# Kernel tuning notes

Measured on AMD Instinct MI355X. Metric: run time of the kernel, lower is better.

## Reference

```python
import jax, jax.numpy as jnp
import numpy as np

EPS = 1e-3  # keras LayerNormalization default epsilon


def _layernorm(x, gamma, beta):
    mu = jnp.mean(x, axis=-1, keepdims=True)
    var = jnp.mean(jnp.square(x - mu), axis=-1, keepdims=True)
    return (x - mu) * jax.lax.rsqrt(var + EPS) * gamma + beta


def setup_inputs() -> dict:
    key = jax.random.key(0)
    B, T, D, H = 8, 2048, 192, 3
    KD = D           # TalkingHeadsAttention(key_dim=dim, value_dim=dim)
    HID = 4 * D      # mlp_ratio = 4.0
    ks = jax.random.split(key, 12)
    s_in = 0.02
    inp = {
        "x": jax.random.normal(ks[0], (B, T, D), jnp.float32),
        # norm1 / norm2
        "gamma1": jnp.ones((D,), jnp.float32),
        "beta1": jnp.zeros((D,), jnp.float32),
        "gamma2": jnp.ones((D,), jnp.float32),
        "beta2": jnp.zeros((D,), jnp.float32),
        # attention projections (qkv_bias=False -> no biases)
        "wq": jax.random.normal(ks[1], (D, H, KD), jnp.float32) * s_in,
        "wk": jax.random.normal(ks[2], (D, H, KD), jnp.float32) * s_in,
        "wv": jax.random.normal(ks[3], (D, H, KD), jnp.float32) * s_in,
        "wo": jax.random.normal(ks[4], (H, KD, D), jnp.float32) * s_in,
        # talking-heads mixing matrices [H, H]
        "pre_w": jnp.eye(H, dtype=jnp.float32) + jax.random.normal(ks[5], (H, H), jnp.float32) * 0.02,
        "post_w": jnp.eye(H, dtype=jnp.float32) + jax.random.normal(ks[6], (H, H), jnp.float32) * 0.02,
        # MLP (bias=True)
        "w1": jax.random.normal(ks[7], (D, HID), jnp.float32) * s_in,
        "b1": jnp.zeros((HID,), jnp.float32),
        "w2": jax.random.normal(ks[8], (HID, D), jnp.float32) * s_in,
        "b2": jnp.zeros((D,), jnp.float32),
    }
    return inp


def reference(x, gamma1, beta1, gamma2, beta2, wq, wk, wv, wo, pre_w, post_w, w1, b1, w2, b2):
    KD = wq.shape[-1]
    # --- pre-norm + talking-heads attention ---
    n = _layernorm(x, gamma1, beta1)                      # [B,T,D]
    q = jnp.einsum("btd,dhk->bthk", n, wq)               # [B,T,H,KD]
    k = jnp.einsum("bsd,dhk->bshk", n, wk)
    v = jnp.einsum("bsd,dhk->bshk", n, wv)
    scores = jnp.einsum("bthk,bshk->bhts", q, k) / jnp.sqrt(jnp.asarray(KD, x.dtype))
    scores = jnp.einsum("bhts,hg->bgts", scores, pre_w)   # pre-softmax head mix
    probs = jax.nn.softmax(scores, axis=-1)
    probs = jnp.einsum("bhts,hg->bgts", probs, post_w)    # post-softmax head mix
    ctx = jnp.einsum("bhts,bshk->bthk", probs, v)         # [B,T,H,KD]
    attn_out = jnp.einsum("bthk,hkd->btd", ctx, wo)       # [B,T,D]
    x = x + attn_out                                      # ls1/drop_path1 are Identity
    # --- pre-norm + MLP ---
    n2 = _layernorm(x, gamma2, beta2)
    h = jax.nn.gelu(n2 @ w1 + b1, approximate=False)      # keras gelu = exact erf
    mlp_out = h @ w2 + b2
    return x + mlp_out
```

## Files before the change

kernel.cpp:

```cpp
#include <hip/hip_runtime.h>
#include <hip/hip_bf16.h>

typedef __hip_bfloat16 bf16;
typedef unsigned char u8;
typedef __attribute__((ext_vector_type(8))) __bf16 bf16x8;
typedef __attribute__((ext_vector_type(4))) float f32x4;
typedef __attribute__((ext_vector_type(2))) float f32x2;

__device__ __forceinline__ void gld_lds16(const void* g, void* l) {
  __builtin_amdgcn_global_load_lds((const __attribute__((address_space(1))) void*)g,
                                   (__attribute__((address_space(3))) void*)l, 16, 0, 0);
}
__device__ __forceinline__ u8 f2e4m3(float v) {
  return (u8)(__builtin_amdgcn_cvt_pk_fp8_f32(v, 0.f, 0, false) & 0xff);
}
__device__ __forceinline__ f32x2 pk_mul(f32x2 a, f32x2 b) {
  f32x2 d;
  asm("v_pk_mul_f32 %0, %1, %2" : "=v"(d) : "v"(a), "v"(b));
  return d;
}
__device__ __forceinline__ f32x2 pk_fma(f32x2 a, f32x2 b, f32x2 c) {
  f32x2 d;
  asm("v_pk_fma_f32 %0, %1, %2, %3" : "=v"(d) : "v"(a), "v"(b), "v"(c));
  return d;
}

__global__ __launch_bounds__(256) void setup_k(
    const float* __restrict__ x, const float* __restrict__ gamma1, const float* __restrict__ beta1,
    const float* __restrict__ wq, const float* __restrict__ wk,
    const float* __restrict__ wv, const float* __restrict__ wo,
    const float* __restrict__ post_w, const float* __restrict__ w1, const float* __restrict__ w2,
    bf16* __restrict__ nb, bf16* __restrict__ WqkvT,
    bf16* __restrict__ w1f, bf16* __restrict__ w2f)
{
  const int bid = blockIdx.x;
  if (bid < 432) {
    const int j = bid * 256 + threadIdx.x;
    const int dd = j % 192;
    const int r = j / 192;
    const int h = r / 192, din = r % 192;
    float acc = 0.f;
    #pragma unroll
    for (int g2 = 0; g2 < 3; ++g2) {
      const float pw = post_w[h*3 + g2];
      const float* wvp = wv + (size_t)din*576 + g2*192;
      const float* wop = wo + (size_t)(g2*192)*192 + dd;
      float s0 = 0.f, s1 = 0.f, s2 = 0.f, s3 = 0.f;
      for (int kd = 0; kd < 192; kd += 4) {
        s0 += wvp[kd]     * wop[(size_t)kd*192];
        s1 += wvp[kd + 1] * wop[(size_t)(kd + 1)*192];
        s2 += wvp[kd + 2] * wop[(size_t)(kd + 2)*192];
        s3 += wvp[kd + 3] * wop[(size_t)(kd + 3)*192];
      }
      acc += pw * ((s0 + s1) + (s2 + s3));
    }
    WqkvT[(size_t)(1152 + h*192 + dd)*192 + din] = __float2bfloat16(acc);
    return;
  }
  if (bid < 2448) {
    int i = (bid - 432) * 256 + threadIdx.x;
    if (i < 221184) {
      int n = i / 192, d = i % 192;
      int sel = n / 576, c = n % 576, h = c / 192, kd = c % 192;
      const float* w = (sel == 0) ? wq : wk;
      WqkvT[i] = __float2bfloat16(w[(d*3 + h)*192 + kd]);
      return;
    }
    i -= 221184;
    if (i < 147456) {
      int j = i / 192, k = i % 192;
      int c = j >> 6, jc = j & 63, jb = jc >> 4, j15 = jc & 15;
      int kq = k >> 5, sl = (k & 31) >> 3, e7 = k & 7;
      w1f[(size_t)(((c*6 + kq)*4 + jb)*512) + (j15 + (sl << 4))*8 + e7] =
          __float2bfloat16(w1[(size_t)k*768 + j]);
      return;
    }
    i -= 147456;
    {
      int j = i / 192, d = i % 192;
      int c = j >> 6, ks = (j >> 5) & 1, l4 = (j >> 3) & 3, e = j & 7;
      int dn = d >> 4, l15 = d & 15;
      w2f[(size_t)((((c*2 + ks)*12 + dn)*64) + l4*16 + l15)*8 + e] =
          __float2bfloat16(w2[(size_t)j*192 + d]);
    }
    return;
  }
  {
    int row = (bid - 2448) * 4 + (threadIdx.x >> 6);
    int lane = threadIdx.x & 63;
    const float* xr = x + (size_t)row * 192;
    float v0 = xr[lane], v1 = xr[lane + 64], v2 = xr[lane + 128];
    float s = v0 + v1 + v2;
    #pragma unroll
    for (int o = 32; o; o >>= 1) s += __shfl_xor(s, o);
    float mu = s * (1.f / 192.f);
    float d0 = v0 - mu, d1 = v1 - mu, d2 = v2 - mu;
    float q = d0*d0 + d1*d1 + d2*d2;
    #pragma unroll
    for (int o = 32; o; o >>= 1) q += __shfl_xor(q, o);
    float rs = rsqrtf(q * (1.f / 192.f) + 1e-3f);
    bf16* orow = nb + (size_t)row * 192;
    orow[lane]       = __float2bfloat16(d0*rs*gamma1[lane]       + beta1[lane]);
    orow[lane + 64]  = __float2bfloat16(d1*rs*gamma1[lane + 64]  + beta1[lane + 64]);
    orow[lane + 128] = __float2bfloat16(d2*rs*gamma1[lane + 128] + beta1[lane + 128]);
  }
}

__global__ __launch_bounds__(256) void gemm_qkv(
    const bf16* __restrict__ A, const bf16* __restrict__ BT,
    u8* __restrict__ q_out, u8* __restrict__ k_out, u8* __restrict__ mt_out)
{
  const int K = 192;
  const int tid = threadIdx.x, lane = tid & 63, wid = tid >> 6;
  const int l15 = lane & 15, l4 = lane >> 4;
  const int wm = wid >> 1, wn = wid & 1;
  const int row0 = blockIdx.y * 128, col0 = blockIdx.x * 64;
  const int sel0 = col0 / 576;
  __shared__ __align__(16) bf16 As[2][128 * 32];
  __shared__ __align__(16) bf16 Bs[2][64 * 32];
  f32x4 acc[4][2] = {};

#define STAGE(buf_, kt_) do { \
    const bf16* Ab_ = A + (size_t)row0 * K + (kt_) * 32; \
    int c0_ = tid, r0_ = c0_ >> 2, cc0_ = (c0_ & 3) << 3; \
    gld_lds16(Ab_ + (size_t)r0_ * K + cc0_, &As[buf_][c0_ * 8]); \
    int c1_ = tid + 256, r1_ = c1_ >> 2, cc1_ = (c1_ & 3) << 3; \
    gld_lds16(Ab_ + (size_t)r1_ * K + cc1_, &As[buf_][c1_ * 8]); \
    const bf16* Bb_ = BT + (size_t)col0 * K + (kt_) * 32; \
    gld_lds16(Bb_ + (size_t)(tid >> 2) * K + ((tid & 3) << 3), &Bs[buf_][tid * 8]); \
  } while (0)

  STAGE(0, 0);
  for (int kt = 0; kt < 6; ++kt) {
    __syncthreads();
    const int buf = kt & 1;
    if (kt + 1 < 6) STAGE(buf ^ 1, kt + 1);
    const int koff = l4 * 8;
    bf16x8 af[4], bfr[2];
    #pragma unroll
    for (int m = 0; m < 4; ++m)
      af[m] = *(const bf16x8*)&As[buf][(wm*64 + m*16 + l15)*32 + koff];
    #pragma unroll
    for (int n = 0; n < 2; ++n)
      bfr[n] = *(const bf16x8*)&Bs[buf][(wn*32 + n*16 + l15)*32 + koff];
    if (sel0 < 2) {
      #pragma unroll
      for (int m = 0; m < 4; ++m)
        #pragma unroll
        for (int n = 0; n < 2; ++n)
          acc[m][n] = __builtin_amdgcn_mfma_f32_16x16x32_bf16(bfr[n], af[m], acc[m][n], 0, 0, 0);
    } else {
      #pragma unroll
      for (int m = 0; m < 4; ++m)
        #pragma unroll
        for (int n = 0; n < 2; ++n)
          acc[m][n] = __builtin_amdgcn_mfma_f32_16x16x32_bf16(af[m], bfr[n], acc[m][n], 0, 0, 0);
    }
  }
#undef STAGE

  if (sel0 < 2) {
    u8* dst = (sel0 == 0) ? q_out : k_out;
    #pragma unroll
    for (int m = 0; m < 4; ++m) {
      const int t = row0 + wm*64 + m*16 + l15;
      const int b = t >> 11, t2 = t & 2047;
      #pragma unroll
      for (int n = 0; n < 2; ++n) {
        const int c2 = (col0 - sel0*576) + wn*32 + n*16 + l4*4;
        const int h = c2 / 192, kd = c2 % 192;
        int pk = __builtin_amdgcn_cvt_pk_fp8_f32(acc[m][n][0], acc[m][n][1], 0, false);
        pk = __builtin_amdgcn_cvt_pk_fp8_f32(acc[m][n][2], acc[m][n][3], pk, true);
        const size_t fo = ((((size_t)b*64 + (t2>>5))*3 + h)*6 + (kd>>5))*1024
                        + (((t2>>4)&1))*512
                        + (((t2&15) + (((kd>>3)&3)<<4))<<3) + (kd&7);
        *(unsigned*)&dst[fo] = (unsigned)pk;
      }
    }
  } else {
    const int rbase = row0 + wm * 64;
    const int cbase = col0 + wn * 32;
    #pragma unroll
    for (int m = 0; m < 4; ++m) {
      #pragma unroll
      for (int n = 0; n < 2; ++n) {
        const int col = cbase + n*16 + l15;
        const int rtop = rbase + m*16 + (l4 << 2);
        const int b = rtop >> 11, t_ = rtop & 2047;
        const int c2 = col % 576;
        const int h = c2 / 192, kd = c2 % 192;
        int pk = __builtin_amdgcn_cvt_pk_fp8_f32(acc[m][n][0], acc[m][n][1], 0, false);
        pk = __builtin_amdgcn_cvt_pk_fp8_f32(acc[m][n][2], acc[m][n][3], pk, true);
        const size_t fo = ((((size_t)b*64 + (t_>>5))*3 + h)*12 + (kd>>4))*512
                        + (((kd&15) + (((t_>>3)&3)<<4))<<3) + (t_&4);
        *(unsigned*)&mt_out[fo] = (unsigned)pk;
      }
    }
  }
}

__global__ __launch_bounds__(256, 2) void attn_k(
    const u8* __restrict__ q, const u8* __restrict__ kf,
    const u8* __restrict__ MT, const float* __restrict__ pre_w,
    const float* __restrict__ x, const float* __restrict__ gamma2,
    const float* __restrict__ beta2, const bf16* __restrict__ w1f,
    const bf16* __restrict__ w2f, const float* __restrict__ b1,
    const float* __restrict__ b2, float* __restrict__ out)
{
  const int tid = threadIdx.x, lane = tid & 63, wv = tid >> 6;
  const int l15 = lane & 15, l4 = lane >> 4;
  const int tq = wv & 1, sq = wv >> 1;
  const int bid = blockIdx.x;
  const int b = bid & 7;
  const int tt = bid >> 3;
  const int t0 = tt * 32;

  __shared__ __align__(16) u8 S[43008];
  __shared__ float rlPart[2][3][32];
  __shared__ float lnS[4][32][2];
  u8* KsP = S;
  u8* PsP = S + 36864;
  bf16* N2 = (bf16*)S;
  bf16* BsP = (bf16*)(S + 12800);
  bf16* Hf = (bf16*)(S + 37376);

  const u8* qfb = q + ((size_t)b*64 + tt) * 18432;
  long qf[3][6];
  #pragma unroll
  for (int h = 0; h < 3; ++h)
    #pragma unroll
    for (int kq = 0; kq < 6; ++kq)
      qf[h][kq] = *(const long*)(qfb + ((h*6 + kq)*2 + tq)*512 + lane*8);

  f32x2 pwf2[9];
  #pragma unroll
  for (int i = 0; i < 9; ++i) {
    const float v = pre_w[i] * 0.07216878364870323f * 1.44269504088896f;
    pwf2[i][0] = v; pwf2[i][1] = v;
  }

  f32x4 acc[3][2][3] = {};
  float sgacc[3] = {0.f, 0.f, 0.f};
  const int trow = tq*16 + l15;
  const int psw = (l15 >> 2) & 3;
  const int pwr = (((sq*2 + (l4 >> 1)) ^ psw) << 3) + ((l4 & 1) << 2);
  const int prd = (l4 ^ psw) << 3;

  const u8* kfb = kf + (size_t)b * 64 * 18432;
  const u8* mtb = MT + (size_t)b * 64 * 18432;

#define STAGEK(buf_, st_) do { \
    const u8* kb_ = kfb + (size_t)(st_) * 18432; \
    _Pragma("unroll") \
    for (int i_ = 0; i_ < 5; ++i_) { \
      const int L_ = i_ * 256 + tid; \
      if (L_ < 1152) gld_lds16(kb_ + L_*16, KsP + (buf_)*18432 + L_*16); \
    } \
  } while (0)

#define LOADMF(MF_, st_) do { \
    const u8* mb_ = mtb + (size_t)(st_) * 18432 + wv*3*512 + lane*8; \
    _Pragma("unroll") \
    for (int g_ = 0; g_ < 3; ++g_) \
      _Pragma("unroll") \
      for (int n_ = 0; n_ < 3; ++n_) \
        MF_[g_][n_] = *(const long*)(mb_ + (g_*12 + n_)*512); \
  } while (0)

#define PV(stm1_, MF_) do { \
    const int bp_ = (stm1_) & 1; \
    __builtin_amdgcn_s_setprio(1); \
    _Pragma("unroll") \
    for (int g_ = 0; g_ < 3; ++g_) \
      _Pragma("unroll") \
      for (int m_ = 0; m_ < 2; ++m_) { \
        const long pf_ = *(const long*)(PsP + bp_*3072 + g_*1024 + (m_*16 + l15)*32 + prd); \
        _Pragma("unroll") \
        for (int n_ = 0; n_ < 3; ++n_) \
          acc[g_][m_][n_] = __builtin_amdgcn_mfma_f32_16x16x32_fp8_fp8(pf_, MF_[g_][n_], acc[g_][m_][n_], 0, 0, 0); \
      } \
    __builtin_amdgcn_s_setprio(0); \
  } while (0)

#define QKSM(st_) do { \
    const int bq_ = (st_) & 1; \
    f32x4 sacc0 = {}, sacc1 = {}, sacc2 = {}; \
    __builtin_amdgcn_s_setprio(1); \
    _Pragma("unroll") \
    for (int kq_ = 0; kq_ < 6; ++kq_) { \
      const long kf0_ = *(const long*)(KsP + bq_*18432 + (((0*6 + kq_)*2 + sq)*512) + lane*8); \
      sacc0 = __builtin_amdgcn_mfma_f32_16x16x32_fp8_fp8(kf0_, qf[0][kq_], sacc0, 0, 0, 0); \
      const long kf1_ = *(const long*)(KsP + bq_*18432 + (((1*6 + kq_)*2 + sq)*512) + lane*8); \
      sacc1 = __builtin_amdgcn_mfma_f32_16x16x32_fp8_fp8(kf1_, qf[1][kq_], sacc1, 0, 0, 0); \
      const long kf2_ = *(const long*)(KsP + bq_*18432 + (((2*6 + kq_)*2 + sq)*512) + lane*8); \
      sacc2 = __builtin_amdgcn_mfma_f32_16x16x32_fp8_fp8(kf2_, qf[2][kq_], sacc2, 0, 0, 0); \
    } \
    __builtin_amdgcn_s_setprio(0); \
    f32x2 p0a = {sacc0[0], sacc0[1]}, p0b = {sacc0[2], sacc0[3]}; \
    f32x2 p1a = {sacc1[0], sacc1[1]}, p1b = {sacc1[2], sacc1[3]}; \
    f32x2 p2a = {sacc2[0], sacc2[1]}, p2b = {sacc2[2], sacc2[3]}; \
    _Pragma("unroll") \
    for (int g_ = 0; g_ < 3; ++g_) { \
      f32x2 va = pk_mul(p0a, pwf2[g_]); \
      va = pk_fma(p1a, pwf2[3+g_], va); \
      va = pk_fma(p2a, pwf2[6+g_], va); \
      f32x2 vb = pk_mul(p0b, pwf2[g_]); \
      vb = pk_fma(p1b, pwf2[3+g_], vb); \
      vb = pk_fma(p2b, pwf2[6+g_], vb); \
      float e0_ = exp2f(va[0]), e1_ = exp2f(va[1]); \
      float e2_ = exp2f(vb[0]), e3_ = exp2f(vb[1]); \
      sgacc[g_] += (e0_ + e1_) + (e2_ + e3_); \
      int pk_ = __builtin_amdgcn_cvt_pk_fp8_f32(e0_, e1_, 0, false); \
      pk_ = __builtin_amdgcn_cvt_pk_fp8_f32(e2_, e3_, pk_, true); \
      *(unsigned*)(PsP + bq_*3072 + g_*1024 + trow*32 + pwr) = (unsigned)pk_; \
    } \
  } while (0)

#define STAGEB(c_) do { \
    const u8* wsrc_ = (const u8*)w1f + (size_t)(c_) * 24576; \
    _Pragma("unroll") \
    for (int i_ = 0; i_ < 6; ++i_) { \
      const int L_ = i_ * 256 + tid; \
      gld_lds16(wsrc_ + L_*16, (u8*)BsP + L_*16); \
    } \
  } while (0)

  long mfA[3][3], mfB[3][3];

  STAGEK(0, 0);
  __syncthreads();
  STAGEK(1, 1);
  LOADMF(mfA, 0);
  QKSM(0);
  for (int st = 1; st < 63; st += 2) {
    __syncthreads();
    STAGEK((st + 1) & 1, st + 1);
    LOADMF(mfB, st);
    PV(st - 1, mfA);
    QKSM(st);
    __syncthreads();
    if (st + 2 < 64) STAGEK((st + 2) & 1, st + 2);
    LOADMF(mfA, st + 1);
    PV(st, mfB);
    QKSM(st + 1);
  }
  __syncthreads();
  LOADMF(mfB, 63);
  PV(62, mfA);
  QKSM(63);
  __syncthreads();
  PV(63, mfB);
  STAGEB(0);
  #pragma unroll
  for (int g = 0; g < 3; ++g) {
    float s = sgacc[g];
    s += __shfl_xor(s, 16);
    s += __shfl_xor(s, 32);
    if (l4 == 0) rlPart[sq][g][trow] = s;
  }
  __syncthreads();

  float ovv[2][3][4];
  #pragma unroll
  for (int m = 0; m < 2; ++m) {
    #pragma unroll
    for (int j = 0; j < 4; ++j) {
      const int row = m*16 + l4*4 + j;
      float rlv[3];
      #pragma unroll
      for (int g = 0; g < 3; ++g)
        rlv[g] = 1.f / (rlPart[0][g][row] + rlPart[1][g][row]);
      float s = 0.f, ss = 0.f;
      #pragma unroll
      for (int n = 0; n < 3; ++n) {
        const int d = wv*48 + n*16 + l15;
        const size_t idx = ((size_t)b*2048 + t0 + row)*192 + d;
        const float ov = x[idx] + rlv[0]*acc[0][m][n][j] + rlv[1]*acc[1][m][n][j]
                                + rlv[2]*acc[2][m][n][j];
        ovv[m][n][j] = ov;
        s += ov; ss += ov*ov;
      }
      #pragma unroll
      for (int o = 1; o < 16; o <<= 1) { s += __shfl_xor(s, o); ss += __shfl_xor(ss, o); }
      if (l15 == 0) { lnS[wv][row][0] = s; lnS[wv][row][1] = ss; }
    }
  }
  __syncthreads();

  {
    float gmL[3], btL[3];
    #pragma unroll
    for (int n = 0; n < 3; ++n) {
      const int d = wv*48 + n*16 + l15;
      gmL[n] = gamma2[d]; btL[n] = beta2[d];
    }
    #pragma unroll
    for (int m = 0; m < 2; ++m) {
      #pragma unroll
      for (int j = 0; j < 4; ++j) {
        const int row = m*16 + l4*4 + j;
        const float ts  = lnS[0][row][0] + lnS[1][row][0] + lnS[2][row][0] + lnS[3][row][0];
        const float tss = lnS[0][row][1] + lnS[1][row][1] + lnS[2][row][1] + lnS[3][row][1];
        const float mu = ts * (1.f / 192.f);
        const float rs = rsqrtf(tss * (1.f / 192.f) - mu*mu + 1e-3f);
        #pragma unroll
        for (int n = 0; n < 3; ++n) {
          const int d = wv*48 + n*16 + l15;
          N2[(((d>>5)*2 + m)*512) + (((row&15) + (((d&31)>>3)<<4))<<3) + (d&7)] =
              __float2bfloat16((ovv[m][n][j] - mu) * rs * gmL[n] + btL[n]);
        }
      }
    }
  }
  __syncthreads();

  const int wm = wv >> 1, wn = wv & 1;
  f32x4 macc[2][3] = {};
  for (int c = 0; c < 12; ++c) {
    bf16x8 wf[3][2];
    #pragma unroll
    for (int n = 0; n < 3; ++n)
      #pragma unroll
      for (int ks = 0; ks < 2; ++ks)
        wf[n][ks] = *(const bf16x8*)(w2f + (size_t)((((c*2 + ks)*12) + wv*3 + n)*64 + lane)*8);

    f32x4 sacc[2] = {};
    #pragma unroll
    for (int kq = 0; kq < 6; ++kq) {
      const bf16x8 af = *(const bf16x8*)&N2[((kq*2 + wm)*512) + lane*8];
      #pragma unroll
      for (int n = 0; n < 2; ++n) {
        const bf16x8 bfr = *(const bf16x8*)&BsP[((kq*4 + wn*2 + n)*512) + lane*8];
        sacc[n] = __builtin_amdgcn_mfma_f32_16x16x32_bf16(af, bfr, sacc[n], 0, 0, 0);
      }
    }
    #pragma unroll
    for (int n = 0; n < 2; ++n) {
      const int jc = wn*32 + n*16 + l15;
      const float bv = b1[c*64 + jc];
      const int sl = (jc & 31) >> 3, e7 = jc & 7;
      #pragma unroll
      for (int jr = 0; jr < 4; ++jr) {
        const int r15 = l4*4 + jr;
        const float u = sacc[n][jr] + bv;
        const float g = 0.5f * u * (1.f + erff(u * 0.70710678118654752f));
        Hf[((wn*2 + wm)*512) + ((r15 + (sl << 4)) << 3) + e7] = __float2bfloat16(g);
      }
    }
    __syncthreads();
    if (c + 1 < 12) STAGEB(c + 1);
    #pragma unroll
    for (int ks = 0; ks < 2; ++ks) {
      bf16x8 ha[2];
      #pragma unroll
      for (int m = 0; m < 2; ++m)
        ha[m] = *(const bf16x8*)&Hf[((ks*2 + m)*512) + lane*8];
      #pragma unroll
      for (int m = 0; m < 2; ++m)
        #pragma unroll
        for (int n = 0; n < 3; ++n)
          macc[m][n] = __builtin_amdgcn_mfma_f32_16x16x32_bf16(ha[m], wf[n][ks], macc[m][n], 0, 0, 0);
    }
    __syncthreads();
  }

  #pragma unroll
  for (int n = 0; n < 3; ++n) {
    const int d = wv*48 + n*16 + l15;
    const float b2v = b2[d];
    #pragma unroll
    for (int m = 0; m < 2; ++m) {
      #pragma unroll
      for (int jr = 0; jr < 4; ++jr) {
        const int row = m*16 + l4*4 + jr;
        const size_t idx = ((size_t)b*2048 + t0 + row)*192 + d;
        out[idx] = ovv[m][n][jr] + macc[m][n][jr] + b2v;
      }
    }
  }
#undef STAGEK
#undef LOADMF
#undef PV
#undef QKSM
#undef STAGEB
}

extern "C" void kernel_launch(void* const* d_in, const int* in_sizes, int n_in,
                              void* d_out, int out_size, void* d_ws, size_t ws_size,
                              hipStream_t stream)
{
  (void)in_sizes; (void)n_in; (void)out_size; (void)ws_size;
  const float* x      = (const float*)d_in[0];
  const float* gamma1 = (const float*)d_in[1];
  const float* beta1  = (const float*)d_in[2];
  const float* gamma2 = (const float*)d_in[3];
  const float* beta2  = (const float*)d_in[4];
  const float* wq     = (const float*)d_in[5];
  const float* wk     = (const float*)d_in[6];
  const float* wv     = (const float*)d_in[7];
  const float* wo     = (const float*)d_in[8];
  const float* pre_w  = (const float*)d_in[9];
  const float* post_w = (const float*)d_in[10];
  const float* w1     = (const float*)d_in[11];
  const float* b1     = (const float*)d_in[12];
  const float* w2     = (const float*)d_in[13];
  const float* b2     = (const float*)d_in[14];
  float* out = (float*)d_out;

  uint8_t* base = (uint8_t*)d_ws;
  size_t off = 0;
  auto alloc = [&](size_t bytes) {
    uint8_t* r = base + off; off += (bytes + 255) & ~(size_t)255; return r;
  };
  bf16* nb      = (bf16*)alloc((size_t)16384 * 192 * 2);
  u8*   qb      = (u8*)alloc((size_t)9437184);
  u8*   kb      = (u8*)alloc((size_t)9437184);
  u8*   MTslab  = (u8*)alloc((size_t)9437184);
  bf16* WqkvT   = (bf16*)alloc((size_t)331776 * 2);
  bf16* w1f     = (bf16*)alloc((size_t)147456 * 2);
  bf16* w2f     = (bf16*)alloc((size_t)147456 * 2);

  setup_k<<<6544, 256, 0, stream>>>(x, gamma1, beta1, wq, wk, wv, wo, post_w, w1, w2,
                                    nb, WqkvT, w1f, w2f);
  gemm_qkv<<<dim3(27, 128, 1), 256, 0, stream>>>(nb, WqkvT, qb, kb, MTslab);
  attn_k<<<512, 256, 0, stream>>>(qb, kb, MTslab, pre_w, x, gamma2, beta2,
                                  w1f, w2f, b1, b2, out);
}
```

Baseline: 162.7 us.

## Double-buffer W1 staging and GELU tile to pipeline the fused MLP loop

```diff
diff --git a/kernel.cpp b/kernel.cpp
--- a/kernel.cpp
+++ b/kernel.cpp
@@ -215,14 +215,14 @@
   const int tt = bid >> 3;
   const int t0 = tt * 32;
 
-  __shared__ __align__(16) u8 S[43008];
+  __shared__ __align__(16) u8 S[69632];
   __shared__ float rlPart[2][3][32];
   __shared__ float lnS[4][32][2];
   u8* KsP = S;
   u8* PsP = S + 36864;
   bf16* N2 = (bf16*)S;
-  bf16* BsP = (bf16*)(S + 12800);
-  bf16* Hf = (bf16*)(S + 37376);
+  bf16* BsP = (bf16*)(S + 12288);
+  bf16* HfP = (bf16*)(S + 61440);
 
   const u8* qfb = q + ((size_t)b*64 + tt) * 18432;
   long qf[3][6];
@@ -316,12 +316,63 @@
     } \
   } while (0)
 
-#define STAGEB(c_) do { \
+#define STAGEB(buf_, c_) do { \
     const u8* wsrc_ = (const u8*)w1f + (size_t)(c_) * 24576; \
     _Pragma("unroll") \
     for (int i_ = 0; i_ < 6; ++i_) { \
       const int L_ = i_ * 256 + tid; \
-      gld_lds16(wsrc_ + L_*16, (u8*)BsP + L_*16); \
+      gld_lds16(wsrc_ + L_*16, (u8*)BsP + (buf_)*24576 + L_*16); \
+    } \
+  } while (0)
+
+#define LOADWF(WF_, c_) do { \
+    _Pragma("unroll") \
+    for (int n_ = 0; n_ < 3; ++n_) \
+      _Pragma("unroll") \
+      for (int ks_ = 0; ks_ < 2; ++ks_) \
+        WF_[n_][ks_] = *(const bf16x8*)(w2f + (size_t)(((((c_)*2 + ks_)*12) + wv*3 + n_)*64 + lane)*8); \
+  } while (0)
+
+  const int wmm = wv >> 1, wnn = wv & 1;
+
+#define MGEMM1(c_) do { \
+    f32x4 sacc[2] = {}; \
+    _Pragma("unroll") \
+    for (int kq_ = 0; kq_ < 6; ++kq_) { \
+      const bf16x8 af_ = *(const bf16x8*)&N2[((kq_*2 + wmm)*512) + lane*8]; \
+      _Pragma("unroll") \
+      for (int n_ = 0; n_ < 2; ++n_) { \
+        const bf16x8 bfr_ = *(const bf16x8*)&BsP[((c_)&1)*12288 + ((kq_*4 + wnn*2 + n_)*512) + lane*8]; \
+        sacc[n_] = __builtin_amdgcn_mfma_f32_16x16x32_bf16(af_, bfr_, sacc[n_], 0, 0, 0); \
+      } \
+    } \
+    _Pragma("unroll") \
+    for (int n_ = 0; n_ < 2; ++n_) { \
+      const int jc_ = wnn*32 + n_*16 + l15; \
+      const float bv_ = b1[(c_)*64 + jc_]; \
+      const int sl_ = (jc_ & 31) >> 3, e7_ = jc_ & 7; \
+      _Pragma("unroll") \
+      for (int jr_ = 0; jr_ < 4; ++jr_) { \
+        const int r15_ = l4*4 + jr_; \
+        const float u_ = sacc[n_][jr_] + bv_; \
+        const float g_ = 0.5f * u_ * (1.f + erff(u_ * 0.70710678118654752f)); \
+        HfP[((c_)&1)*2048 + ((wnn*2 + wmm)*512) + ((r15_ + (sl_ << 4)) << 3) + e7_] = __float2bfloat16(g_); \
+      } \
+    } \
+  } while (0)
+
+#define MGEMM2(WF_, hbuf_) do { \
+    _Pragma("unroll") \
+    for (int ks_ = 0; ks_ < 2; ++ks_) { \
+      bf16x8 ha_[2]; \
+      _Pragma("unroll") \
+      for (int m_ = 0; m_ < 2; ++m_) \
+        ha_[m_] = *(const bf16x8*)&HfP[(hbuf_)*2048 + ((ks_*2 + m_)*512) + lane*8]; \
+      _Pragma("unroll") \
+      for (int m_ = 0; m_ < 2; ++m_) \
+        _Pragma("unroll") \
+        for (int n_ = 0; n_ < 3; ++n_) \
+          macc[m_][n_] = __builtin_amdgcn_mfma_f32_16x16x32_bf16(ha_[m_], WF_[n_][ks_], macc[m_][n_], 0, 0, 0); \
     } \
   } while (0)
 
@@ -350,7 +401,7 @@
   QKSM(63);
   __syncthreads();
   PV(63, mfB);
-  STAGEB(0);
+  STAGEB(0, 0);
   #pragma unroll
   for (int g = 0; g < 3; ++g) {
     float s = sgacc[g];
@@ -358,6 +409,16 @@
     s += __shfl_xor(s, 32);
     if (l4 == 0) rlPart[sq][g][trow] = s;
   }
+  float xv[2][3][4];
+  #pragma unroll
+  for (int m = 0; m < 2; ++m)
+    #pragma unroll
+    for (int n = 0; n < 3; ++n) {
+      const int d = wv*48 + n*16 + l15;
+      #pragma unroll
+      for (int j = 0; j < 4; ++j)
+        xv[m][n][j] = x[((size_t)b*2048 + t0 + m*16 + l4*4 + j)*192 + d];
+    }
   __syncthreads();
 
   float ovv[2][3][4];
@@ -373,10 +434,8 @@
       float s = 0.f, ss = 0.f;
       #pragma unroll
       for (int n = 0; n < 3; ++n) {
-        const int d = wv*48 + n*16 + l15;
-        const size_t idx = ((size_t)b*2048 + t0 + row)*192 + d;
-        const float ov = x[idx] + rlv[0]*acc[0][m][n][j] + rlv[1]*acc[1][m][n][j]
-                                + rlv[2]*acc[2][m][n][j];
+        const float ov = xv[m][n][j] + rlv[0]*acc[0][m][n][j] + rlv[1]*acc[1][m][n][j]
+                                     + rlv[2]*acc[2][m][n][j];
         ovv[m][n][j] = ov;
         s += ov; ss += ov*ov;
       }
@@ -414,55 +473,30 @@
   }
   __syncthreads();
 
-  const int wm = wv >> 1, wn = wv & 1;
   f32x4 macc[2][3] = {};
-  for (int c = 0; c < 12; ++c) {
-    bf16x8 wf[3][2];
-    #pragma unroll
-    for (int n = 0; n < 3; ++n)
-      #pragma unroll
-      for (int ks = 0; ks < 2; ++ks)
-        wf[n][ks] = *(const bf16x8*)(w2f + (size_t)((((c*2 + ks)*12) + wv*3 + n)*64 + lane)*8);
-
-    f32x4 sacc[2] = {};
-    #pragma unroll
-    for (int kq = 0; kq < 6; ++kq) {
-      const bf16x8 af = *(const bf16x8*)&N2[((kq*2 + wm)*512) + lane*8];
-      #pragma unroll
-      for (int n = 0; n < 2; ++n) {
-        const bf16x8 bfr = *(const bf16x8*)&BsP[((kq*4 + wn*2 + n)*512) + lane*8];
-        sacc[n] = __builtin_amdgcn_mfma_f32_16x16x32_bf16(af, bfr, sacc[n], 0, 0, 0);
-      }
-    }
-    #pragma unroll
-    for (int n = 0; n < 2; ++n) {
-      const int jc = wn*32 + n*16 + l15;
-      const float bv = b1[c*64 + jc];
-      const int sl = (jc & 31) >> 3, e7 = jc & 7;
-      #pragma unroll
-      for (int jr = 0; jr < 4; ++jr) {
-        const int r15 = l4*4 + jr;
-        const float u = sacc[n][jr] + bv;
-        const float g = 0.5f * u * (1.f + erff(u * 0.70710678118654752f));
-        Hf[((wn*2 + wm)*512) + ((r15 + (sl << 4)) << 3) + e7] = __float2bfloat16(g);
-      }
-    }
+  bf16x8 wfA[3][2], wfB[3][2];
+
+  STAGEB(1, 1);
+  LOADWF(wfA, 0);
+  MGEMM1(0);
+  __syncthreads();
+  for (int c = 1; c < 11; c += 2) {
+    STAGEB((c + 1) & 1, c + 1);
+    LOADWF(wfB, c);
+    MGEMM2(wfA, (c - 1) & 1);
+    MGEMM1(c);
     __syncthreads();
-    if (c + 1 < 12) STAGEB(c + 1);
-    #pragma unroll
-    for (int ks = 0; ks < 2; ++ks) {
-      bf16x8 ha[2];
-      #pragma unroll
-      for (int m = 0; m < 2; ++m)
-        ha[m] = *(const bf16x8*)&Hf[((ks*2 + m)*512) + lane*8];
-      #pragma unroll
-      for (int m = 0; m < 2; ++m)
-        #pragma unroll
-        for (int n = 0; n < 3; ++n)
-          macc[m][n] = __builtin_amdgcn_mfma_f32_16x16x32_bf16(ha[m], wf[n][ks], macc[m][n], 0, 0, 0);
-    }
+    if (c + 2 < 12) STAGEB((c + 2) & 1, c + 2);
+    LOADWF(wfA, c + 1);
+    MGEMM2(wfB, c & 1);
+    MGEMM1(c + 1);
     __syncthreads();
   }
+  LOADWF(wfB, 11);
+  MGEMM2(wfA, 0);
+  MGEMM1(11);
+  __syncthreads();
+  MGEMM2(wfB, 1);
 
   #pragma unroll
   for (int n = 0; n < 3; ++n) {
@@ -483,6 +517,9 @@
 #undef PV
 #undef QKSM
 #undef STAGEB
+#undef LOADWF
+#undef MGEMM1
+#undef MGEMM2
 }
 
 extern "C" void kernel_launch(void* const* d_in, const int* in_sizes, int n_in,
```

Result: no change. 161.4 us, median of 2 (-0.8%).
